# Optimization experiments

Hardware: AMD Instinct MI355X
Metric: run time of the kernel (lower is better)

## Reference

```python
import jax, jax.numpy as jnp
from jax import lax
import numpy as np

B, T, C, H = 1024, 512, 32, 256


def _gru_cell(x, h, Wih, Whh, bih, bhh):
    # PyTorch GRU gate math. x: (B, C_in), h: (B, H)
    gi = x @ Wih.T + bih          # (B, 3H)
    gh = h @ Whh.T + bhh          # (B, 3H)
    i_r, i_z, i_n = jnp.split(gi, 3, axis=-1)
    h_r, h_z, h_n = jnp.split(gh, 3, axis=-1)
    r = jax.nn.sigmoid(i_r + h_r)
    z = jax.nn.sigmoid(i_z + h_z)
    n = jnp.tanh(i_n + r * h_n)
    return (1.0 - z) * n + z * h


def setup_inputs() -> dict:
    key = jax.random.key(0)
    ks = jax.random.split(key, 12)
    s = 0.08  # ~ uniform(-1/sqrt(H)) scale
    return {
        "x": jax.random.normal(ks[0], (B, T, C), dtype=jnp.float32),
        "enc_Wih": jax.random.normal(ks[1], (3 * H, C), dtype=jnp.float32) * s,
        "enc_Whh": jax.random.normal(ks[2], (3 * H, H), dtype=jnp.float32) * s,
        "enc_bih": jax.random.normal(ks[3], (3 * H,), dtype=jnp.float32) * s,
        "enc_bhh": jax.random.normal(ks[4], (3 * H,), dtype=jnp.float32) * s,
        "dec_Wih": jax.random.normal(ks[5], (3 * H, C), dtype=jnp.float32) * s,
        "dec_Whh": jax.random.normal(ks[6], (3 * H, H), dtype=jnp.float32) * s,
        "dec_bih": jax.random.normal(ks[7], (3 * H,), dtype=jnp.float32) * s,
        "dec_bhh": jax.random.normal(ks[8], (3 * H,), dtype=jnp.float32) * s,
        "proj_W": jax.random.normal(ks[9], (C, H), dtype=jnp.float32) * s,
        "proj_b": jax.random.normal(ks[10], (C,), dtype=jnp.float32) * s,
    }


def reference(x, enc_Wih, enc_Whh, enc_bih, enc_bhh,
              dec_Wih, dec_Whh, dec_bih, dec_bhh, proj_W, proj_b):
    batch = x.shape[0]
    h0 = jnp.zeros((batch, H), dtype=x.dtype)

    # ---- encoder: scan over time, keep only final hidden ----
    xs = jnp.swapaxes(x, 0, 1)  # (T, B, C)

    def enc_step(h, xt):
        return _gru_cell(xt, h, enc_Wih, enc_Whh, enc_bih, enc_bhh), None

    h_enc, _ = lax.scan(enc_step, h0, xs)

    start = jnp.zeros((batch, C), dtype=x.dtype)

    def dec_step(carry, _):
        h, prev = carry
        h_new = _gru_cell(prev, h, dec_Wih, dec_Whh, dec_bih, dec_bhh)
        pred = h_new @ proj_W.T + proj_b  # (B, C)
        return (h_new, pred), pred

    _, preds = lax.scan(dec_step, (h_enc, start), None, length=T)
    return jnp.swapaxes(preds, 0, 1)  # (B, T, C)
```

## Files before the change

kernel.cpp:

```cpp
#include <hip/hip_runtime.h>

typedef short bf16x8 __attribute__((ext_vector_type(8)));
typedef float f32x4 __attribute__((ext_vector_type(4)));

#define MFMA16(a, b, c) __builtin_amdgcn_mfma_f32_16x16x32_bf16(a, b, c, 0, 0, 0)

#define T_ 512
#define C_ 32
#define H_ 256

__device__ __forceinline__ unsigned short f2bf(float f) {
  union { float f; unsigned u; } v; v.f = f;
  return (unsigned short)((v.u + 0x7fffu + ((v.u >> 16) & 1u)) >> 16);
}

__global__ void pack_kernel(
    const float* __restrict__ encWih, const float* __restrict__ encWhh,
    const float* __restrict__ encbih, const float* __restrict__ encbhh,
    const float* __restrict__ decWih, const float* __restrict__ decWhh,
    const float* __restrict__ decbih, const float* __restrict__ decbhh,
    const float* __restrict__ projW, const float* __restrict__ projB,
    unsigned short* __restrict__ encW, unsigned short* __restrict__ decW,
    unsigned short* __restrict__ pW, float* __restrict__ encBias,
    float* __restrict__ decBias, float* __restrict__ pB) {
  const float SRZ = -1.442695041f;
  const float SN  = 2.885390082f;
  int i = blockIdx.x * 256 + threadIdx.x;
  if (i < 768 * 288) {
    int n = i / 288, k = i % 288;
    float sc = (n < 512) ? SRZ : SN;
    float ve = (k < 32) ? encWih[n * 32 + k] : encWhh[n * 256 + k - 32];
    float vd = (k < 32) ? decWih[n * 32 + k] : decWhh[n * 256 + k - 32];
    encW[i] = f2bf(ve * sc);
    decW[i] = f2bf(vd * sc);
  }
  if (i < 32 * 256) pW[i] = f2bf(projW[i]);
  if (i < 256) {
    encBias[i]       = (encbih[i] + encbhh[i]) * SRZ;
    encBias[256 + i] = (encbih[256 + i] + encbhh[256 + i]) * SRZ;
    encBias[512 + i] = encbih[512 + i] * SN;
    encBias[768 + i] = encbhh[512 + i] * SN;
    decBias[i]       = (decbih[i] + decbhh[i]) * SRZ;
    decBias[256 + i] = (decbih[256 + i] + decbhh[256 + i]) * SRZ;
    decBias[512 + i] = decbih[512 + i] * SN;
    decBias[768 + i] = decbhh[512 + i] * SN;
  }
  if (i < 32) pB[i] = projB[i];
}

__global__ __launch_bounds__(1024) void gru_kernel(
    const float* __restrict__ x,
    const unsigned short* __restrict__ encW,
    const unsigned short* __restrict__ decW,
    const unsigned short* __restrict__ pW,
    const float* __restrict__ encBias,
    const float* __restrict__ decBias,
    const float* __restrict__ pB,
    float* __restrict__ out) {
  __shared__ __align__(16) unsigned short wnl[6][256][40];
  __shared__ __align__(16) unsigned short h_lds[2][16][264];
  __shared__ __align__(16) unsigned short xb[2][16][40];
  __shared__ __align__(16) unsigned short pwl[32][264];

  const int tid = (int)threadIdx.x;
  const int wave = tid >> 6, lane = tid & 63;
  const int l15 = lane & 15, l4 = lane >> 4;
  const int ko = l4 * 8;
  const int aswz = ((l4 + (l15 >> 2)) & 3) << 3;
  const int gbase = (int)blockIdx.x * 16;
  const int j = wave * 16 + l15;
  const int jswz = (j & ~31) | ((((j >> 3) + l4) & 3) << 3) | (j & 7);

  for (int i = tid; i < 2 * 16 * 264 / 2; i += 1024) ((unsigned*)h_lds)[i] = 0;
  for (int i = tid; i < 2 * 16 * 40 / 2; i += 1024) ((unsigned*)xb)[i] = 0;
  {
    int n = tid >> 5, slot = tid & 31;
    *(bf16x8*)&pwl[n][slot * 8] = *(const bf16x8*)(pW + n * 256 + slot * 8);
  }

  const int sg = tid >> 5, sc = tid & 31;
  const int scswz = ((((sc >> 3) + (sg >> 2)) & 3) << 3) | (sc & 7);
  const float* xLane = x + (size_t)(gbase + sg) * (T_ * C_) + sc;
  float* outLane = out + (size_t)(gbase + l4 * 4) * (T_ * C_) + wave * 16 + l15;
  const float pbias = (wave < 2) ? pB[wave * 16 + l15] : 0.f;
  const int nswz = ((((l15 >> 3) + l4) & 3) << 3) | (l15 & 7);
  f32x4 hreg = {0.f, 0.f, 0.f, 0.f};

  bf16x8 wi0, wi1, wi2, wr[8], wz[8], wn2[2];

  auto loadW = [&](const unsigned short* Wp) {
    wi0 = *(const bf16x8*)(Wp + (size_t)j * 288 + ko);
    wi1 = *(const bf16x8*)(Wp + (size_t)(j + 256) * 288 + ko);
    wi2 = *(const bf16x8*)(Wp + (size_t)(j + 512) * 288 + ko);
#pragma unroll
    for (int kk = 0; kk < 8; ++kk) {
      wr[kk] = *(const bf16x8*)(Wp + (size_t)j * 288 + 32 + kk * 32 + ko);
      wz[kk] = *(const bf16x8*)(Wp + (size_t)(j + 256) * 288 + 32 + kk * 32 + ko);
    }
#pragma unroll
    for (int kk = 0; kk < 2; ++kk)
      wn2[kk] = *(const bf16x8*)(Wp + (size_t)(j + 512) * 288 + 32 + kk * 32 + ko);
    for (int i = tid; i < 6 * 256 * 4; i += 1024) {
      int kc = i >> 10, rem = i & 1023;
      int jj = rem >> 2, kc2 = rem & 3;
      *(bf16x8*)&wnl[kc][jj][kc2 * 8] =
          *(const bf16x8*)(Wp + (size_t)(jj + 512) * 288 + 32 + (kc + 2) * 32 + kc2 * 8);
    }
  };

  auto gates_store = [&](const f32x4& accr, const f32x4& accz,
                         const f32x4& accin, const f32x4& acchn, int buf) {
#pragma unroll
    for (int r = 0; r < 4; ++r) {
      float rg = __builtin_amdgcn_rcpf(1.0f + __builtin_amdgcn_exp2f(accr[r]));
      float zg = __builtin_amdgcn_rcpf(1.0f + __builtin_amdgcn_exp2f(accz[r]));
      float ng = 1.0f - 2.0f * __builtin_amdgcn_rcpf(
                              1.0f + __builtin_amdgcn_exp2f(accin[r] + rg * acchn[r]));
      float h = zg * (hreg[r] - ng) + ng;
      hreg[r] = h;
      h_lds[buf][l4 * 4 + r][jswz] = f2bf(h);
    }
  };

  loadW(encW);
  float br = encBias[j], bz = encBias[256 + j];
  float bin = encBias[512 + j], bhn = encBias[768 + j];
  if (tid < 512) xb[0][sg][scswz] = f2bf(xLane[0]);
  __syncthreads();

  for (int t = 0; t < T_; ++t) {
    if (t < T_ - 1 && tid < 512)
      xb[(t + 1) & 1][sg][scswz] = f2bf(xLane[(size_t)(t + 1) * C_]);

    f32x4 accr = {br, br, br, br}, accz = {bz, bz, bz, bz};
    f32x4 accin = {bin, bin, bin, bin}, acchn = {bhn, bhn, bhn, bhn};
    {
      bf16x8 a0 = *(const bf16x8*)&xb[t & 1][l15][aswz];
      accr  = MFMA16(a0, wi0, accr);
      accz  = MFMA16(a0, wi1, accz);
      accin = MFMA16(a0, wi2, accin);
    }
#pragma unroll
    for (int kk = 0; kk < 8; ++kk) {
      bf16x8 ah = *(const bf16x8*)&h_lds[t & 1][l15][kk * 32 + aswz];
      accr = MFMA16(ah, wr[kk], accr);
      accz = MFMA16(ah, wz[kk], accz);
      bf16x8 wnk = (kk < 2) ? wn2[kk] : *(const bf16x8*)&wnl[kk - 2][j][ko];
      acchn = MFMA16(ah, wnk, acchn);
    }
    gates_store(accr, accz, accin, acchn, (t + 1) & 1);
    __syncthreads();
  }

  loadW(decW);
  br = decBias[j]; bz = decBias[256 + j];
  bin = decBias[512 + j]; bhn = decBias[768 + j];
  if (tid < 320) ((unsigned*)xb)[tid] = 0;
  __syncthreads();

  const int pn = wave * 16 + l15;
  const int pnswz = ((((pn >> 3) + l4) & 3) << 3) | (pn & 7);

  for (int t = 0; t < T_; ++t) {
    f32x4 accr = {br, br, br, br}, accz = {bz, bz, bz, bz};
    f32x4 accin = {bin, bin, bin, bin}, acchn = {bhn, bhn, bhn, bhn};
    {
      bf16x8 a0 = *(const bf16x8*)&xb[0][l15][aswz];
      accr  = MFMA16(a0, wi0, accr);
      accz  = MFMA16(a0, wi1, accz);
      accin = MFMA16(a0, wi2, accin);
    }
#pragma unroll
    for (int kk = 0; kk < 8; ++kk) {
      bf16x8 ah = *(const bf16x8*)&h_lds[t & 1][l15][kk * 32 + aswz];
      accr = MFMA16(ah, wr[kk], accr);
      accz = MFMA16(ah, wz[kk], accz);
      bf16x8 wnk = (kk < 2) ? wn2[kk] : *(const bf16x8*)&wnl[kk - 2][j][ko];
      acchn = MFMA16(ah, wnk, acchn);
    }
    gates_store(accr, accz, accin, acchn, (t + 1) & 1);
    __syncthreads();

    if (wave < 2) {
      f32x4 pa = {pbias, pbias, pbias, pbias};
#pragma unroll
      for (int kk = 0; kk < 8; ++kk) {
        bf16x8 ah = *(const bf16x8*)&h_lds[(t + 1) & 1][l15][kk * 32 + aswz];
        bf16x8 bw = *(const bf16x8*)&pwl[pn][kk * 32 + ko];
        pa = MFMA16(ah, bw, pa);
      }
#pragma unroll
      for (int r = 0; r < 4; ++r) {
        outLane[(size_t)r * (T_ * C_) + t * C_] = pa[r];
        xb[0][l4 * 4 + r][pnswz] = f2bf(pa[r]);
      }
    }
    __syncthreads();
  }
}

extern "C" void kernel_launch(void* const* d_in, const int* in_sizes, int n_in,
                              void* d_out, int out_size, void* d_ws, size_t ws_size,
                              hipStream_t stream) {
  const float* x      = (const float*)d_in[0];
  const float* encWih = (const float*)d_in[1];
  const float* encWhh = (const float*)d_in[2];
  const float* encbih = (const float*)d_in[3];
  const float* encbhh = (const float*)d_in[4];
  const float* decWih = (const float*)d_in[5];
  const float* decWhh = (const float*)d_in[6];
  const float* decbih = (const float*)d_in[7];
  const float* decbhh = (const float*)d_in[8];
  const float* projW  = (const float*)d_in[9];
  const float* projB  = (const float*)d_in[10];

  char* ws = (char*)d_ws;
  unsigned short* encW = (unsigned short*)(ws);
  unsigned short* decW = (unsigned short*)(ws + 442368);
  unsigned short* pW   = (unsigned short*)(ws + 884736);
  float* encBias = (float*)(ws + 901120);
  float* decBias = (float*)(ws + 905216);
  float* pB      = (float*)(ws + 909312);

  pack_kernel<<<864, 256, 0, stream>>>(encWih, encWhh, encbih, encbhh,
                                       decWih, decWhh, decbih, decbhh,
                                       projW, projB,
                                       encW, decW, pW, encBias, decBias, pB);
  gru_kernel<<<64, 1024, 0, stream>>>(x, encW, decW, pW, encBias, decBias, pB,
                                      (float*)d_out);
}
```

Before: 2.665 ms.

## Keep all recurrent weights in registers and move input weights to LDS

All three hidden-to-hidden weight blocks (r, z, n) now stay in registers for every k-chunk, so the n-gate weights are no longer read from LDS on each timestep. The small input-weight blocks move into LDS in their place. The XOR-style swizzles on the h, x and projection LDS buffers are also removed in favour of plain indexing. This cuts LDS traffic in the recurrent inner loop, at the cost of higher register pressure and possible LDS bank conflicts from the unswizzled layout.

```diff
diff --git a/kernel.cpp b/kernel.cpp
--- a/kernel.cpp
+++ b/kernel.cpp
@@ -57,7 +57,7 @@
     const float* __restrict__ decBias,
     const float* __restrict__ pB,
     float* __restrict__ out) {
-  __shared__ __align__(16) unsigned short wnl[6][256][40];
+  __shared__ __align__(16) unsigned short wih[3][256][40];
   __shared__ __align__(16) unsigned short h_lds[2][16][264];
   __shared__ __align__(16) unsigned short xb[2][16][40];
   __shared__ __align__(16) unsigned short pwl[32][264];
@@ -66,10 +66,8 @@
   const int wave = tid >> 6, lane = tid & 63;
   const int l15 = lane & 15, l4 = lane >> 4;
   const int ko = l4 * 8;
-  const int aswz = ((l4 + (l15 >> 2)) & 3) << 3;
   const int gbase = (int)blockIdx.x * 16;
   const int j = wave * 16 + l15;
-  const int jswz = (j & ~31) | ((((j >> 3) + l4) & 3) << 3) | (j & 7);
 
   for (int i = tid; i < 2 * 16 * 264 / 2; i += 1024) ((unsigned*)h_lds)[i] = 0;
   for (int i = tid; i < 2 * 16 * 40 / 2; i += 1024) ((unsigned*)xb)[i] = 0;
@@ -78,33 +76,25 @@
     *(bf16x8*)&pwl[n][slot * 8] = *(const bf16x8*)(pW + n * 256 + slot * 8);
   }
 
-  const int sg = tid >> 5, sc = tid & 31;
-  const int scswz = ((((sc >> 3) + (sg >> 2)) & 3) << 3) | (sc & 7);
-  const float* xLane = x + (size_t)(gbase + sg) * (T_ * C_) + sc;
+  const float* xLane = x + (size_t)(gbase + (tid >> 5)) * (T_ * C_) + (tid & 31);
   float* outLane = out + (size_t)(gbase + l4 * 4) * (T_ * C_) + wave * 16 + l15;
   const float pbias = (wave < 2) ? pB[wave * 16 + l15] : 0.f;
-  const int nswz = ((((l15 >> 3) + l4) & 3) << 3) | (l15 & 7);
   f32x4 hreg = {0.f, 0.f, 0.f, 0.f};
 
-  bf16x8 wi0, wi1, wi2, wr[8], wz[8], wn2[2];
+  bf16x8 wr[8], wz[8], wn[8];
 
   auto loadW = [&](const unsigned short* Wp) {
-    wi0 = *(const bf16x8*)(Wp + (size_t)j * 288 + ko);
-    wi1 = *(const bf16x8*)(Wp + (size_t)(j + 256) * 288 + ko);
-    wi2 = *(const bf16x8*)(Wp + (size_t)(j + 512) * 288 + ko);
 #pragma unroll
     for (int kk = 0; kk < 8; ++kk) {
       wr[kk] = *(const bf16x8*)(Wp + (size_t)j * 288 + 32 + kk * 32 + ko);
       wz[kk] = *(const bf16x8*)(Wp + (size_t)(j + 256) * 288 + 32 + kk * 32 + ko);
-    }
-#pragma unroll
-    for (int kk = 0; kk < 2; ++kk)
-      wn2[kk] = *(const bf16x8*)(Wp + (size_t)(j + 512) * 288 + 32 + kk * 32 + ko);
-    for (int i = tid; i < 6 * 256 * 4; i += 1024) {
-      int kc = i >> 10, rem = i & 1023;
-      int jj = rem >> 2, kc2 = rem & 3;
-      *(bf16x8*)&wnl[kc][jj][kc2 * 8] =
-          *(const bf16x8*)(Wp + (size_t)(jj + 512) * 288 + 32 + (kc + 2) * 32 + kc2 * 8);
+      wn[kk] = *(const bf16x8*)(Wp + (size_t)(j + 512) * 288 + 32 + kk * 32 + ko);
+    }
+    for (int i = tid; i < 3072; i += 1024) {
+      int g = i >> 10, rem = i & 1023;
+      int row = rem >> 2, kc = rem & 3;
+      *(bf16x8*)&wih[g][row][kc * 8] =
+          *(const bf16x8*)(Wp + (size_t)(g * 256 + row) * 288 + kc * 8);
     }
   };
 
@@ -118,35 +108,34 @@
                               1.0f + __builtin_amdgcn_exp2f(accin[r] + rg * acchn[r]));
       float h = zg * (hreg[r] - ng) + ng;
       hreg[r] = h;
-      h_lds[buf][l4 * 4 + r][jswz] = f2bf(h);
+      h_lds[buf][l4 * 4 + r][j] = f2bf(h);
     }
   };
 
   loadW(encW);
   float br = encBias[j], bz = encBias[256 + j];
   float bin = encBias[512 + j], bhn = encBias[768 + j];
-  if (tid < 512) xb[0][sg][scswz] = f2bf(xLane[0]);
+  if (tid < 512) xb[0][tid >> 5][tid & 31] = f2bf(xLane[0]);
   __syncthreads();
 
   for (int t = 0; t < T_; ++t) {
     if (t < T_ - 1 && tid < 512)
-      xb[(t + 1) & 1][sg][scswz] = f2bf(xLane[(size_t)(t + 1) * C_]);
+      xb[(t + 1) & 1][tid >> 5][tid & 31] = f2bf(xLane[(size_t)(t + 1) * C_]);
 
     f32x4 accr = {br, br, br, br}, accz = {bz, bz, bz, bz};
     f32x4 accin = {bin, bin, bin, bin}, acchn = {bhn, bhn, bhn, bhn};
     {
-      bf16x8 a0 = *(const bf16x8*)&xb[t & 1][l15][aswz];
-      accr  = MFMA16(a0, wi0, accr);
-      accz  = MFMA16(a0, wi1, accz);
-      accin = MFMA16(a0, wi2, accin);
+      bf16x8 a0 = *(const bf16x8*)&xb[t & 1][l15][ko];
+      accr  = MFMA16(a0, *(const bf16x8*)&wih[0][j][ko], accr);
+      accz  = MFMA16(a0, *(const bf16x8*)&wih[1][j][ko], accz);
+      accin = MFMA16(a0, *(const bf16x8*)&wih[2][j][ko], accin);
     }
 #pragma unroll
     for (int kk = 0; kk < 8; ++kk) {
-      bf16x8 ah = *(const bf16x8*)&h_lds[t & 1][l15][kk * 32 + aswz];
-      accr = MFMA16(ah, wr[kk], accr);
-      accz = MFMA16(ah, wz[kk], accz);
-      bf16x8 wnk = (kk < 2) ? wn2[kk] : *(const bf16x8*)&wnl[kk - 2][j][ko];
-      acchn = MFMA16(ah, wnk, acchn);
+      bf16x8 ah = *(const bf16x8*)&h_lds[t & 1][l15][kk * 32 + ko];
+      accr  = MFMA16(ah, wr[kk], accr);
+      accz  = MFMA16(ah, wz[kk], accz);
+      acchn = MFMA16(ah, wn[kk], acchn);
     }
     gates_store(accr, accz, accin, acchn, (t + 1) & 1);
     __syncthreads();
@@ -158,41 +147,38 @@
   if (tid < 320) ((unsigned*)xb)[tid] = 0;
   __syncthreads();
 
-  const int pn = wave * 16 + l15;
-  const int pnswz = ((((pn >> 3) + l4) & 3) << 3) | (pn & 7);
-
   for (int t = 0; t < T_; ++t) {
     f32x4 accr = {br, br, br, br}, accz = {bz, bz, bz, bz};
     f32x4 accin = {bin, bin, bin, bin}, acchn = {bhn, bhn, bhn, bhn};
     {
-      bf16x8 a0 = *(const bf16x8*)&xb[0][l15][aswz];
-      accr  = MFMA16(a0, wi0, accr);
-      accz  = MFMA16(a0, wi1, accz);
-      accin = MFMA16(a0, wi2, accin);
+      bf16x8 a0 = *(const bf16x8*)&xb[0][l15][ko];
+      accr  = MFMA16(a0, *(const bf16x8*)&wih[0][j][ko], accr);
+      accz  = MFMA16(a0, *(const bf16x8*)&wih[1][j][ko], accz);
+      accin = MFMA16(a0, *(const bf16x8*)&wih[2][j][ko], accin);
     }
 #pragma unroll
     for (int kk = 0; kk < 8; ++kk) {
-      bf16x8 ah = *(const bf16x8*)&h_lds[t & 1][l15][kk * 32 + aswz];
-      accr = MFMA16(ah, wr[kk], accr);
-      accz = MFMA16(ah, wz[kk], accz);
-      bf16x8 wnk = (kk < 2) ? wn2[kk] : *(const bf16x8*)&wnl[kk - 2][j][ko];
-      acchn = MFMA16(ah, wnk, acchn);
+      bf16x8 ah = *(const bf16x8*)&h_lds[t & 1][l15][kk * 32 + ko];
+      accr  = MFMA16(ah, wr[kk], accr);
+      accz  = MFMA16(ah, wz[kk], accz);
+      acchn = MFMA16(ah, wn[kk], acchn);
     }
     gates_store(accr, accz, accin, acchn, (t + 1) & 1);
     __syncthreads();
 
     if (wave < 2) {
       f32x4 pa = {pbias, pbias, pbias, pbias};
+      const int pn = wave * 16 + l15;
 #pragma unroll
       for (int kk = 0; kk < 8; ++kk) {
-        bf16x8 ah = *(const bf16x8*)&h_lds[(t + 1) & 1][l15][kk * 32 + aswz];
+        bf16x8 ah = *(const bf16x8*)&h_lds[(t + 1) & 1][l15][kk * 32 + ko];
         bf16x8 bw = *(const bf16x8*)&pwl[pn][kk * 32 + ko];
         pa = MFMA16(ah, bw, pa);
       }
 #pragma unroll
       for (int r = 0; r < 4; ++r) {
         outLane[(size_t)r * (T_ * C_) + t * C_] = pa[r];
-        xb[0][l4 * 4 + r][pnswz] = f2bf(pa[r]);
+        xb[0][l4 * 4 + r][pn] = f2bf(pa[r]);
       }
     }
     __syncthreads();
```

Measured after the change: 3.638 ms. +36.5%, slower.
